# Optimization experiments

Measured on AMD Instinct MI355X. Metric: run time of the kernel, lower is better.

## Reference

```python
import jax, jax.numpy as jnp
import numpy as np

D = 2048
H = 16
HD = 128
INNER = H * HD
EPS = 1e-6


def rmsnorm(x, w):
    var = jnp.mean(x * x, axis=-1, keepdims=True)
    return x * jax.lax.rsqrt(var + EPS) * w


def setup_inputs() -> dict:
    key = jax.random.key(0)
    ks = jax.random.split(key, 10)
    B, T, N_ws, T_corr = 2, 2048, 64, 512
    scale = 1.0 / np.sqrt(D)
    return {
        "hidden_states": jax.random.normal(ks[0], (B, T, D), jnp.float32),
        "workspace": jax.random.normal(ks[1], (B, N_ws, D), jnp.float32),
        "correction_tokens": jax.random.normal(ks[2], (B, T_corr, D), jnp.float32),
        "correction_mask": jax.random.randint(ks[3], (B, T_corr), 0, 2, jnp.int32),
        "ln_q_w": jnp.ones((D,), jnp.float32),
        "ln_kv_w": jnp.ones((D,), jnp.float32),
        "Wq": jax.random.normal(ks[4], (D, INNER), jnp.float32) * scale,
        "Wk": jax.random.normal(ks[5], (D, INNER), jnp.float32) * scale,
        "Wv": jax.random.normal(ks[6], (D, INNER), jnp.float32) * scale,
        "Wo": jax.random.normal(ks[7], (INNER, D), jnp.float32) * scale,
    }


def reference(hidden_states, workspace, correction_tokens, correction_mask,
              ln_q_w, ln_kv_w, Wq, Wk, Wv, Wo):
    B, T, _ = hidden_states.shape
    N_ws = workspace.shape[1]
    # kv context = [workspace ; correction_tokens]
    kv_context = jnp.concatenate([workspace, correction_tokens], axis=1)  # (B, N_kv, D)
    N_kv = kv_context.shape[1]
    ws_mask = jnp.ones((B, N_ws), hidden_states.dtype)
    kv_mask = jnp.concatenate([ws_mask, correction_mask.astype(hidden_states.dtype)], axis=1)  # (B, N_kv)

    h = rmsnorm(hidden_states, ln_q_w)
    kv = rmsnorm(kv_context, ln_kv_w)

    q = (h @ Wq).reshape(B, T, H, HD)        # (B,T,H,hd)
    k = (kv @ Wk).reshape(B, N_kv, H, HD)
    v = (kv @ Wv).reshape(B, N_kv, H, HD)

    scores = jnp.einsum("bthd,bshd->bhts", q, k) / np.sqrt(HD)  # (B,H,T,N_kv)
    mask = (kv_mask != 0)[:, None, None, :]                      # (B,1,1,N_kv)
    scores = jnp.where(mask, scores, -jnp.inf)
    attn = jax.nn.softmax(scores, axis=-1)
    attn = jnp.nan_to_num(attn, nan=0.0)
    # dropout is identity in eval mode
    out = jnp.einsum("bhts,bshd->bthd", attn, v).reshape(B, T, INNER)
    return out @ Wo
```

## Files before the change

### kernel.cpp

```cpp
#include <hip/hip_runtime.h>
#include <hip/hip_bf16.h>
#include <math.h>

typedef __bf16 bf16;
typedef __attribute__((ext_vector_type(8))) __bf16 bf16x8;
typedef __attribute__((ext_vector_type(4))) __bf16 bf16x4;
typedef __attribute__((ext_vector_type(4))) float f32x4;

#define D_DIM 2048
#define NKV   576

__device__ inline void gld_lds16(const void* g, void* l) {
    void* gg = const_cast<void*>(g);
    __builtin_amdgcn_global_load_lds(
        (__attribute__((address_space(1))) void*)gg,
        (__attribute__((address_space(3))) void*)l, 16, 0, 0);
}

__global__ __launch_bounds__(256) void proj_all(
    const bf16* __restrict__ hb, const bf16* __restrict__ kvb,
    const bf16* __restrict__ WqT, const bf16* __restrict__ WkvT,
    bf16* __restrict__ qb, bf16* __restrict__ kvout)
{
    __shared__ __align__(16) bf16 As[128 * 64];
    __shared__ __align__(16) bf16 Bs[128 * 64];

    int id = blockIdx.x;
    const bf16 *A, *B; bf16* C; int ldc, m0, n0;
    if (id < 512) {
        A = hb; B = WqT; C = qb; ldc = 2048;
        m0 = (id >> 4) * 128; n0 = (id & 15) * 128;
    } else {
        id -= 512;
        A = kvb; B = WkvT; C = kvout; ldc = 4096;
        m0 = (id >> 5) * 128; n0 = (id & 31) * 128;
    }
    const int tid = threadIdx.x, lane = tid & 63;
    const int wm = ((tid >> 6) >> 1) * 64, wn = ((tid >> 6) & 1) * 64;
    const int fr = lane & 15, fg = lane >> 4;

    f32x4 acc[4][4] = {};

    for (int k0 = 0; k0 < 2048; k0 += 64) {
#pragma unroll
        for (int p = 0; p < 4; ++p) {
            const int c = p * 256 + tid;
            const int r = c >> 3, cl = (c & 7) ^ (r & 7);
            gld_lds16(A + (long)(m0 + r) * 2048 + k0 + cl * 8, As + c * 8);
            gld_lds16(B + (long)(n0 + r) * 2048 + k0 + cl * 8, Bs + c * 8);
        }
        __syncthreads();
#pragma unroll
        for (int s = 0; s < 2; ++s) {
            const int sl = ((s << 2) + fg) ^ (fr & 7);
            bf16x8 af[4], bg[4];
#pragma unroll
            for (int i = 0; i < 4; ++i)
                af[i] = *(const bf16x8*)(As + (((wm + i * 16 + fr) << 3) + sl) * 8);
#pragma unroll
            for (int j = 0; j < 4; ++j)
                bg[j] = *(const bf16x8*)(Bs + (((wn + j * 16 + fr) << 3) + sl) * 8);
#pragma unroll
            for (int i = 0; i < 4; ++i)
#pragma unroll
                for (int j = 0; j < 4; ++j)
                    acc[i][j] = __builtin_amdgcn_mfma_f32_16x16x32_bf16(
                        af[i], bg[j], acc[i][j], 0, 0, 0);
        }
        __syncthreads();
    }

    const int er = fg * 4;
#pragma unroll
    for (int i = 0; i < 4; ++i)
#pragma unroll
        for (int j = 0; j < 4; ++j) {
            const int n = n0 + wn + j * 16 + fr;
#pragma unroll
            for (int r = 0; r < 4; ++r)
                C[(long)(m0 + wm + i * 16 + er + r) * ldc + n] = (bf16)acc[i][j][r];
        }
}

__global__ __launch_bounds__(256) void gemm_final(
    const bf16* __restrict__ A, const bf16* __restrict__ B, float* __restrict__ C)
{
    __shared__ __align__(16) bf16 As[128 * 64];
    __shared__ __align__(16) bf16 Bs[128 * 64];

    const int m0 = blockIdx.y * 128, n0 = blockIdx.x * 128;
    const int tid = threadIdx.x, lane = tid & 63;
    const int wm = ((tid >> 6) >> 1) * 64, wn = ((tid >> 6) & 1) * 64;
    const int fr = lane & 15, fg = lane >> 4;

    f32x4 acc[4][4] = {};

    for (int k0 = 0; k0 < 2048; k0 += 64) {
#pragma unroll
        for (int p = 0; p < 4; ++p) {
            const int c = p * 256 + tid;
            const int r = c >> 3, cl = (c & 7) ^ (r & 7);
            gld_lds16(A + (long)(m0 + r) * 2048 + k0 + cl * 8, As + c * 8);
            gld_lds16(B + (long)(n0 + r) * 2048 + k0 + cl * 8, Bs + c * 8);
        }
        __syncthreads();
#pragma unroll
        for (int s = 0; s < 2; ++s) {
            const int sl = ((s << 2) + fg) ^ (fr & 7);
            bf16x8 af[4], bg[4];
#pragma unroll
            for (int i = 0; i < 4; ++i)
                af[i] = *(const bf16x8*)(As + (((wm + i * 16 + fr) << 3) + sl) * 8);
#pragma unroll
            for (int j = 0; j < 4; ++j)
                bg[j] = *(const bf16x8*)(Bs + (((wn + j * 16 + fr) << 3) + sl) * 8);
#pragma unroll
            for (int i = 0; i < 4; ++i)
#pragma unroll
                for (int j = 0; j < 4; ++j)
                    acc[i][j] = __builtin_amdgcn_mfma_f32_16x16x32_bf16(
                        af[i], bg[j], acc[i][j], 0, 0, 0);
        }
        __syncthreads();
    }

    const int er = fg * 4;
#pragma unroll
    for (int i = 0; i < 4; ++i)
#pragma unroll
        for (int j = 0; j < 4; ++j) {
            const int n = n0 + wn + j * 16 + fr;
#pragma unroll
            for (int r = 0; r < 4; ++r)
                C[(long)(m0 + wm + i * 16 + er + r) * 2048 + n] = acc[i][j][r];
        }
}

__global__ __launch_bounds__(256) void rmsnorm_all(
    const float* __restrict__ hidden, const float* __restrict__ wsp,
    const float* __restrict__ corr, const float* __restrict__ lnq,
    const float* __restrict__ lnkv, bf16* __restrict__ hb, bf16* __restrict__ kvb)
{
    const int r = blockIdx.x;
    const float* xr; const float* w; bf16* yr;
    if (r < 4096) {
        xr = hidden + (long)r * D_DIM; w = lnq; yr = hb + (long)r * D_DIM;
    } else if (r < 4224) {
        const int rr = r - 4096;
        xr = wsp + (long)rr * D_DIM; w = lnkv;
        yr = kvb + ((long)(rr >> 6) * NKV + (rr & 63)) * D_DIM;
    } else {
        const int rr = r - 4224;
        xr = corr + (long)rr * D_DIM; w = lnkv;
        yr = kvb + ((long)(rr >> 9) * NKV + 64 + (rr & 511)) * D_DIM;
    }
    const int t = threadIdx.x;

    float4 v0 = *(const float4*)(xr + t * 4);
    float4 v1 = *(const float4*)(xr + 1024 + t * 4);
    float ss = v0.x * v0.x + v0.y * v0.y + v0.z * v0.z + v0.w * v0.w
             + v1.x * v1.x + v1.y * v1.y + v1.z * v1.z + v1.w * v1.w;
#pragma unroll
    for (int off = 32; off; off >>= 1) ss += __shfl_xor(ss, off);
    __shared__ float p[4];
    if ((t & 63) == 0) p[t >> 6] = ss;
    __syncthreads();
    const float rs = rsqrtf((p[0] + p[1] + p[2] + p[3]) * (1.0f / 2048.0f) + 1e-6f);

    float4 w0 = *(const float4*)(w + t * 4);
    float4 w1 = *(const float4*)(w + 1024 + t * 4);
    bf16x4 o0 = { (bf16)(v0.x * rs * w0.x), (bf16)(v0.y * rs * w0.y),
                  (bf16)(v0.z * rs * w0.z), (bf16)(v0.w * rs * w0.w) };
    bf16x4 o1 = { (bf16)(v1.x * rs * w1.x), (bf16)(v1.y * rs * w1.y),
                  (bf16)(v1.z * rs * w1.z), (bf16)(v1.w * rs * w1.w) };
    *(bf16x4*)(yr + t * 4) = o0;
    *(bf16x4*)(yr + 1024 + t * 4) = o1;
}

__global__ __launch_bounds__(256) void wcast_t(
    const float* __restrict__ w0, const float* __restrict__ w1,
    const float* __restrict__ w2, const float* __restrict__ w3,
    bf16* __restrict__ o0, bf16* __restrict__ o1,
    bf16* __restrict__ o2, bf16* __restrict__ o3)
{
    const float* in; bf16* out;
    switch (blockIdx.z) {
        case 0:  in = w0; out = o0; break;
        case 1:  in = w1; out = o1; break;
        case 2:  in = w2; out = o2; break;
        default: in = w3; out = o3; break;
    }
    __shared__ float tile[32][33];
    const int t  = threadIdx.x;
    const int r0 = blockIdx.y * 32, c0 = blockIdx.x * 32;
    const int r = t >> 3, c = (t & 7) * 4;
    float4 v = *(const float4*)(in + (long)(r0 + r) * 2048 + c0 + c);
    tile[r][c] = v.x; tile[r][c + 1] = v.y; tile[r][c + 2] = v.z; tile[r][c + 3] = v.w;
    __syncthreads();
    bf16x4 o = { (bf16)tile[c][r], (bf16)tile[c + 1][r],
                 (bf16)tile[c + 2][r], (bf16)tile[c + 3][r] };
    *(bf16x4*)(out + (long)(c0 + r) * 2048 + r0 + c) = o;
}

__global__ __launch_bounds__(256) void vtrans(
    const bf16* __restrict__ kv, bf16* __restrict__ vt)
{
    const int z = blockIdx.z, bb = z >> 4, hh = z & 15;
    __shared__ bf16 tile[32][36];
    const int t  = threadIdx.x;
    const int d0 = blockIdx.x * 32, s0 = blockIdx.y * 32;
    const int r = t >> 3, c = (t & 7) * 4;
    bf16x4 val = *(const bf16x4*)(kv + (long)(bb * NKV + s0 + r) * 4096 + 2048 + hh * 128 + d0 + c);
    tile[r][c] = val[0]; tile[r][c + 1] = val[1];
    tile[r][c + 2] = val[2]; tile[r][c + 3] = val[3];
    __syncthreads();
    bf16x4 o = { tile[c][r], tile[c + 1][r], tile[c + 2][r], tile[c + 3][r] };
    *(bf16x4*)(vt + ((long)z * 128 + d0 + r) * NKV + s0 + c) = o;
}

__global__ __launch_bounds__(256, 4) void flash_attn(
    const bf16* __restrict__ Q, const bf16* __restrict__ KV,
    const bf16* __restrict__ VT, const int* __restrict__ cmask,
    bf16* __restrict__ O)
{
    __shared__ __align__(16) bf16 Ks[64 * 128];
    __shared__ __align__(16) bf16 VTs[128 * 64];

    const int qt = blockIdx.x, h = blockIdx.y, b = blockIdx.z;
    const int tid = threadIdx.x, lane = tid & 63, w = tid >> 6;
    const int fr = lane & 15, fg = lane >> 4;

    const bf16* qbase = Q + ((long)(b * 2048 + qt * 64)) * 2048 + h * 128;
    bf16x8 qf[4];
#pragma unroll
    for (int s = 0; s < 4; ++s)
        qf[s] = *(const bf16x8*)(qbase + (long)(w * 16 + fr) * 2048 + s * 32 + fg * 8);

    float m_r[4], l_r[4];
    f32x4 acc_o[8];
#pragma unroll
    for (int r = 0; r < 4; ++r) { m_r[r] = -3.0e38f; l_r[r] = 0.f; }
#pragma unroll
    for (int j = 0; j < 8; ++j) acc_o[j] = (f32x4){0.f, 0.f, 0.f, 0.f};

    const float scale2 = 0.12752792330124195f;
    const bf16* kbase = KV + (long)b * NKV * 4096 + h * 128;
    const bf16* vbase = VT + ((long)(b * 16 + h)) * 128 * NKV;

    for (int kc = 0; kc < 9; ++kc) {
        const int kv0 = kc * 64;
#pragma unroll
        for (int p = 0; p < 4; ++p) {
            const int c = p * 256 + tid;
            const int r = c >> 4, cs = c & 15, cl = cs ^ (r & 15);
            gld_lds16(kbase + (long)(kv0 + r) * 4096 + cl * 8, Ks + c * 8);
        }
#pragma unroll
        for (int p = 0; p < 4; ++p) {
            const int c = p * 256 + tid;
            const int r = c >> 3, cs = c & 7, cl = cs ^ (r & 7);
            gld_lds16(vbase + (long)r * NKV + kv0 + cl * 8, VTs + c * 8);
        }
        __syncthreads();

        f32x4 acc_s[4] = {};
#pragma unroll
        for (int s = 0; s < 4; ++s) {
#pragma unroll
            for (int j = 0; j < 4; ++j) {
                bf16x8 bg = *(const bf16x8*)(Ks +
                    ((j * 16 + fr) * 16 + ((s * 4 + fg) ^ fr)) * 8);
                acc_s[j] = __builtin_amdgcn_mfma_f32_16x16x32_bf16(qf[s], bg, acc_s[j], 0, 0, 0);
            }
        }

        float bias[4];
#pragma unroll
        for (int j = 0; j < 4; ++j) {
            const int kv = kv0 + j * 16 + fr;
            const bool valid = (kv < 64) || (cmask[b * 512 + kv - 64] != 0);
            bias[j] = valid ? 0.f : -1e30f;
        }
        float s_f[4][4];
        float mc[4] = {-3.0e38f, -3.0e38f, -3.0e38f, -3.0e38f};
#pragma unroll
        for (int j = 0; j < 4; ++j)
#pragma unroll
            for (int r = 0; r < 4; ++r) {
                float v = fmaf(acc_s[j][r], scale2, bias[j]);
                s_f[j][r] = v; mc[r] = fmaxf(mc[r], v);
            }
#pragma unroll
        for (int r = 0; r < 4; ++r) {
            mc[r] = fmaxf(mc[r], __shfl_xor(mc[r], 1));
            mc[r] = fmaxf(mc[r], __shfl_xor(mc[r], 2));
            mc[r] = fmaxf(mc[r], __shfl_xor(mc[r], 4));
            mc[r] = fmaxf(mc[r], __shfl_xor(mc[r], 8));
        }
        float alpha[4];
#pragma unroll
        for (int r = 0; r < 4; ++r) {
            const float mn = fmaxf(m_r[r], mc[r]);
            alpha[r] = __builtin_amdgcn_exp2f(m_r[r] - mn);
            m_r[r] = mn;
        }
        float rs[4] = {0.f, 0.f, 0.f, 0.f};
#pragma unroll
        for (int j = 0; j < 4; ++j)
#pragma unroll
            for (int r = 0; r < 4; ++r) {
                const float pv = __builtin_amdgcn_exp2f(s_f[j][r] - m_r[r]);
                s_f[j][r] = pv; rs[r] += pv;
            }
#pragma unroll
        for (int r = 0; r < 4; ++r) {
            rs[r] += __shfl_xor(rs[r], 1);
            rs[r] += __shfl_xor(rs[r], 2);
            rs[r] += __shfl_xor(rs[r], 4);
            rs[r] += __shfl_xor(rs[r], 8);
            l_r[r] = l_r[r] * alpha[r] + rs[r];
        }
#pragma unroll
        for (int j = 0; j < 8; ++j)
#pragma unroll
            for (int r = 0; r < 4; ++r) acc_o[j][r] *= alpha[r];

        __syncthreads();

        bf16* Ps = Ks;
#pragma unroll
        for (int j = 0; j < 4; ++j)
#pragma unroll
            for (int r = 0; r < 4; ++r)
                Ps[(w * 16 + fg * 4 + r) * 72 + j * 16 + fr] = (bf16)s_f[j][r];

#pragma unroll
        for (int s2 = 0; s2 < 2; ++s2) {
            bf16x8 af = *(const bf16x8*)(Ps + (w * 16 + fr) * 72 + s2 * 32 + fg * 8);
#pragma unroll
            for (int jd = 0; jd < 8; ++jd) {
                bf16x8 bg = *(const bf16x8*)(VTs +
                    ((jd * 16 + fr) * 8 + ((s2 * 4 + fg) ^ (fr & 7))) * 8);
                acc_o[jd] = __builtin_amdgcn_mfma_f32_16x16x32_bf16(af, bg, acc_o[jd], 0, 0, 0);
            }
        }
        __syncthreads();
    }

    bf16* obase = O + ((long)(b * 2048 + qt * 64)) * 2048 + h * 128;
#pragma unroll
    for (int r = 0; r < 4; ++r) {
        const float inv = 1.0f / l_r[r];
        const int row = w * 16 + fg * 4 + r;
#pragma unroll
        for (int jd = 0; jd < 8; ++jd)
            obase[(long)row * 2048 + jd * 16 + fr] = (bf16)(acc_o[jd][r] * inv);
    }
}

extern "C" void kernel_launch(void* const* d_in, const int* in_sizes, int n_in,
                              void* d_out, int out_size, void* d_ws, size_t ws_size,
                              hipStream_t stream)
{
    const float* hidden = (const float*)d_in[0];
    const float* wsp    = (const float*)d_in[1];
    const float* corr   = (const float*)d_in[2];
    const int*   cmask  = (const int*)d_in[3];
    const float* lnq    = (const float*)d_in[4];
    const float* lnkv   = (const float*)d_in[5];
    const float* Wq     = (const float*)d_in[6];
    const float* Wk     = (const float*)d_in[7];
    const float* Wv     = (const float*)d_in[8];
    const float* Wo     = (const float*)d_in[9];
    float* out = (float*)d_out;

    char* ws = (char*)d_ws;
    size_t off = 0;
    auto alloc = [&](size_t sz) { void* p = ws + off; off += (sz + 255) & ~(size_t)255; return p; };

    bf16* WqT   = (bf16*)alloc(2048ull * 2048 * 2);
    bf16* WkvT  = (bf16*)alloc(4096ull * 2048 * 2);
    bf16* WoT   = (bf16*)alloc(2048ull * 2048 * 2);
    bf16* hb    = (bf16*)alloc(4096ull * 2048 * 2);
    bf16* kvb   = (bf16*)alloc(1152ull * 2048 * 2);
    bf16* qb    = (bf16*)alloc(4096ull * 2048 * 2);
    bf16* kvout = (bf16*)alloc(1152ull * 4096 * 2);
    bf16* vtb   = (bf16*)alloc(4096ull * NKV * 2);
    bf16* aob   = (bf16*)alloc(4096ull * 2048 * 2);

    wcast_t<<<dim3(64, 64, 4), 256, 0, stream>>>(
        Wq, Wk, Wv, Wo, WqT, WkvT, WkvT + 2048ull * 2048, WoT);
    rmsnorm_all<<<5248, 256, 0, stream>>>(hidden, wsp, corr, lnq, lnkv, hb, kvb);
    proj_all<<<800, 256, 0, stream>>>(hb, kvb, WqT, WkvT, qb, kvout);
    vtrans<<<dim3(4, 18, 32), 256, 0, stream>>>(kvout, vtb);
    flash_attn<<<dim3(32, 16, 2), 256, 0, stream>>>(qb, kvout, vtb, cmask, aob);
    gemm_final<<<dim3(16, 32), 256, 0, stream>>>(aob, WoT, out);
}
```

Baseline: 331.0 us.

## Fuse weight cast with rmsnorm and fold V transpose into projection epilogue

Merges the weight transpose-cast kernel and the rmsnorm kernel into a single prep launch. The projection GEMM now writes K to its own contiguous buffer and writes V already transposed via an LDS staging tile, which removes the separate vtrans kernel and the extra round trip of V through global memory. This cuts two kernel launches and one intermediate pass, at the cost of a larger shared-memory footprint in the projection kernel and divergent epilogue paths.

```diff
diff --git a/kernel.cpp b/kernel.cpp
--- a/kernel.cpp
+++ b/kernel.cpp
@@ -17,144 +17,53 @@
         (__attribute__((address_space(3))) void*)l, 16, 0, 0);
 }
 
-__global__ __launch_bounds__(256) void proj_all(
-    const bf16* __restrict__ hb, const bf16* __restrict__ kvb,
-    const bf16* __restrict__ WqT, const bf16* __restrict__ WkvT,
-    bf16* __restrict__ qb, bf16* __restrict__ kvout)
-{
-    __shared__ __align__(16) bf16 As[128 * 64];
-    __shared__ __align__(16) bf16 Bs[128 * 64];
-
-    int id = blockIdx.x;
-    const bf16 *A, *B; bf16* C; int ldc, m0, n0;
-    if (id < 512) {
-        A = hb; B = WqT; C = qb; ldc = 2048;
-        m0 = (id >> 4) * 128; n0 = (id & 15) * 128;
-    } else {
-        id -= 512;
-        A = kvb; B = WkvT; C = kvout; ldc = 4096;
-        m0 = (id >> 5) * 128; n0 = (id & 31) * 128;
-    }
-    const int tid = threadIdx.x, lane = tid & 63;
-    const int wm = ((tid >> 6) >> 1) * 64, wn = ((tid >> 6) & 1) * 64;
-    const int fr = lane & 15, fg = lane >> 4;
-
-    f32x4 acc[4][4] = {};
-
-    for (int k0 = 0; k0 < 2048; k0 += 64) {
-#pragma unroll
-        for (int p = 0; p < 4; ++p) {
-            const int c = p * 256 + tid;
-            const int r = c >> 3, cl = (c & 7) ^ (r & 7);
-            gld_lds16(A + (long)(m0 + r) * 2048 + k0 + cl * 8, As + c * 8);
-            gld_lds16(B + (long)(n0 + r) * 2048 + k0 + cl * 8, Bs + c * 8);
-        }
-        __syncthreads();
-#pragma unroll
-        for (int s = 0; s < 2; ++s) {
-            const int sl = ((s << 2) + fg) ^ (fr & 7);
-            bf16x8 af[4], bg[4];
-#pragma unroll
-            for (int i = 0; i < 4; ++i)
-                af[i] = *(const bf16x8*)(As + (((wm + i * 16 + fr) << 3) + sl) * 8);
-#pragma unroll
-            for (int j = 0; j < 4; ++j)
-                bg[j] = *(const bf16x8*)(Bs + (((wn + j * 16 + fr) << 3) + sl) * 8);
-#pragma unroll
-            for (int i = 0; i < 4; ++i)
-#pragma unroll
-                for (int j = 0; j < 4; ++j)
-                    acc[i][j] = __builtin_amdgcn_mfma_f32_16x16x32_bf16(
-                        af[i], bg[j], acc[i][j], 0, 0, 0);
-        }
-        __syncthreads();
-    }
-
-    const int er = fg * 4;
-#pragma unroll
-    for (int i = 0; i < 4; ++i)
-#pragma unroll
-        for (int j = 0; j < 4; ++j) {
-            const int n = n0 + wn + j * 16 + fr;
-#pragma unroll
-            for (int r = 0; r < 4; ++r)
-                C[(long)(m0 + wm + i * 16 + er + r) * ldc + n] = (bf16)acc[i][j][r];
-        }
-}
-
-__global__ __launch_bounds__(256) void gemm_final(
-    const bf16* __restrict__ A, const bf16* __restrict__ B, float* __restrict__ C)
-{
-    __shared__ __align__(16) bf16 As[128 * 64];
-    __shared__ __align__(16) bf16 Bs[128 * 64];
-
-    const int m0 = blockIdx.y * 128, n0 = blockIdx.x * 128;
-    const int tid = threadIdx.x, lane = tid & 63;
-    const int wm = ((tid >> 6) >> 1) * 64, wn = ((tid >> 6) & 1) * 64;
-    const int fr = lane & 15, fg = lane >> 4;
-
-    f32x4 acc[4][4] = {};
-
-    for (int k0 = 0; k0 < 2048; k0 += 64) {
-#pragma unroll
-        for (int p = 0; p < 4; ++p) {
-            const int c = p * 256 + tid;
-            const int r = c >> 3, cl = (c & 7) ^ (r & 7);
-            gld_lds16(A + (long)(m0 + r) * 2048 + k0 + cl * 8, As + c * 8);
-            gld_lds16(B + (long)(n0 + r) * 2048 + k0 + cl * 8, Bs + c * 8);
-        }
-        __syncthreads();
-#pragma unroll
-        for (int s = 0; s < 2; ++s) {
-            const int sl = ((s << 2) + fg) ^ (fr & 7);
-            bf16x8 af[4], bg[4];
-#pragma unroll
-            for (int i = 0; i < 4; ++i)
-                af[i] = *(const bf16x8*)(As + (((wm + i * 16 + fr) << 3) + sl) * 8);
-#pragma unroll
-            for (int j = 0; j < 4; ++j)
-                bg[j] = *(const bf16x8*)(Bs + (((wn + j * 16 + fr) << 3) + sl) * 8);
-#pragma unroll
-            for (int i = 0; i < 4; ++i)
-#pragma unroll
-                for (int j = 0; j < 4; ++j)
-                    acc[i][j] = __builtin_amdgcn_mfma_f32_16x16x32_bf16(
-                        af[i], bg[j], acc[i][j], 0, 0, 0);
-        }
-        __syncthreads();
-    }
-
-    const int er = fg * 4;
-#pragma unroll
-    for (int i = 0; i < 4; ++i)
-#pragma unroll
-        for (int j = 0; j < 4; ++j) {
-            const int n = n0 + wn + j * 16 + fr;
-#pragma unroll
-            for (int r = 0; r < 4; ++r)
-                C[(long)(m0 + wm + i * 16 + er + r) * 2048 + n] = acc[i][j][r];
-        }
-}
-
-__global__ __launch_bounds__(256) void rmsnorm_all(
+__global__ __launch_bounds__(256) void prep(
     const float* __restrict__ hidden, const float* __restrict__ wsp,
     const float* __restrict__ corr, const float* __restrict__ lnq,
-    const float* __restrict__ lnkv, bf16* __restrict__ hb, bf16* __restrict__ kvb)
+    const float* __restrict__ lnkv,
+    const float* __restrict__ Wq, const float* __restrict__ Wk,
+    const float* __restrict__ Wv, const float* __restrict__ Wo,
+    bf16* __restrict__ hb, bf16* __restrict__ kvb,
+    bf16* __restrict__ WqT, bf16* __restrict__ WkvT, bf16* __restrict__ WoT)
 {
-    const int r = blockIdx.x;
+    __shared__ float tile[32][33];
+    __shared__ float p[4];
+    const int id = blockIdx.x, t = threadIdx.x;
+
+    if (id < 16384) {
+        const int wz = id >> 12, wy = (id >> 6) & 63, wx = id & 63;
+        const float* in; bf16* out;
+        switch (wz) {
+            case 0:  in = Wq; out = WqT; break;
+            case 1:  in = Wk; out = WkvT; break;
+            case 2:  in = Wv; out = WkvT + 2048ull * 2048; break;
+            default: in = Wo; out = WoT; break;
+        }
+        const int r0 = wy * 32, c0 = wx * 32;
+        const int r = t >> 3, c = (t & 7) * 4;
+        float4 v = *(const float4*)(in + (long)(r0 + r) * 2048 + c0 + c);
+        tile[r][c] = v.x; tile[r][c + 1] = v.y;
+        tile[r][c + 2] = v.z; tile[r][c + 3] = v.w;
+        __syncthreads();
+        bf16x4 o = { (bf16)tile[c][r], (bf16)tile[c + 1][r],
+                     (bf16)tile[c + 2][r], (bf16)tile[c + 3][r] };
+        *(bf16x4*)(out + (long)(c0 + r) * 2048 + r0 + c) = o;
+        return;
+    }
+
+    const int rr0 = id - 16384;
     const float* xr; const float* w; bf16* yr;
-    if (r < 4096) {
-        xr = hidden + (long)r * D_DIM; w = lnq; yr = hb + (long)r * D_DIM;
-    } else if (r < 4224) {
-        const int rr = r - 4096;
+    if (rr0 < 4096) {
+        xr = hidden + (long)rr0 * D_DIM; w = lnq; yr = hb + (long)rr0 * D_DIM;
+    } else if (rr0 < 4224) {
+        const int rr = rr0 - 4096;
         xr = wsp + (long)rr * D_DIM; w = lnkv;
         yr = kvb + ((long)(rr >> 6) * NKV + (rr & 63)) * D_DIM;
     } else {
-        const int rr = r - 4224;
+        const int rr = rr0 - 4224;
         xr = corr + (long)rr * D_DIM; w = lnkv;
         yr = kvb + ((long)(rr >> 9) * NKV + 64 + (rr & 511)) * D_DIM;
     }
-    const int t = threadIdx.x;
 
     float4 v0 = *(const float4*)(xr + t * 4);
     float4 v1 = *(const float4*)(xr + 1024 + t * 4);
@@ -162,7 +71,6 @@
              + v1.x * v1.x + v1.y * v1.y + v1.z * v1.z + v1.w * v1.w;
 #pragma unroll
     for (int off = 32; off; off >>= 1) ss += __shfl_xor(ss, off);
-    __shared__ float p[4];
     if ((t & 63) == 0) p[t >> 6] = ss;
     __syncthreads();
     const float rs = rsqrtf((p[0] + p[1] + p[2] + p[3]) * (1.0f / 2048.0f) + 1e-6f);
@@ -177,49 +85,155 @@
     *(bf16x4*)(yr + 1024 + t * 4) = o1;
 }
 
-__global__ __launch_bounds__(256) void wcast_t(
-    const float* __restrict__ w0, const float* __restrict__ w1,
-    const float* __restrict__ w2, const float* __restrict__ w3,
-    bf16* __restrict__ o0, bf16* __restrict__ o1,
-    bf16* __restrict__ o2, bf16* __restrict__ o3)
+__global__ __launch_bounds__(256) void proj_all(
+    const bf16* __restrict__ hb, const bf16* __restrict__ kvb,
+    const bf16* __restrict__ WqT, const bf16* __restrict__ WkvT,
+    bf16* __restrict__ qb, bf16* __restrict__ kb, bf16* __restrict__ vtb)
 {
-    const float* in; bf16* out;
-    switch (blockIdx.z) {
-        case 0:  in = w0; out = o0; break;
-        case 1:  in = w1; out = o1; break;
-        case 2:  in = w2; out = o2; break;
-        default: in = w3; out = o3; break;
-    }
-    __shared__ float tile[32][33];
-    const int t  = threadIdx.x;
-    const int r0 = blockIdx.y * 32, c0 = blockIdx.x * 32;
-    const int r = t >> 3, c = (t & 7) * 4;
-    float4 v = *(const float4*)(in + (long)(r0 + r) * 2048 + c0 + c);
-    tile[r][c] = v.x; tile[r][c + 1] = v.y; tile[r][c + 2] = v.z; tile[r][c + 3] = v.w;
+    __shared__ __align__(16) bf16 smem[128 * 132];
+    bf16* As = smem;
+    bf16* Bs = smem + 128 * 64;
+
+    int id = blockIdx.x;
+    const bf16 *A, *B; int m0, n0; bool isQ;
+    if (id < 512) {
+        isQ = true; A = hb; B = WqT;
+        m0 = (id >> 4) * 128; n0 = (id & 15) * 128;
+    } else {
+        id -= 512;
+        isQ = false; A = kvb; B = WkvT;
+        m0 = (id >> 5) * 128; n0 = (id & 31) * 128;
+    }
+    const int tid = threadIdx.x, lane = tid & 63;
+    const int wm = ((tid >> 6) >> 1) * 64, wn = ((tid >> 6) & 1) * 64;
+    const int fr = lane & 15, fg = lane >> 4;
+
+    f32x4 acc[4][4] = {};
+
+    for (int k0 = 0; k0 < 2048; k0 += 64) {
+#pragma unroll
+        for (int p = 0; p < 4; ++p) {
+            const int c = p * 256 + tid;
+            const int r = c >> 3, cl = (c & 7) ^ (r & 7);
+            gld_lds16(A + (long)(m0 + r) * 2048 + k0 + cl * 8, As + c * 8);
+            gld_lds16(B + (long)(n0 + r) * 2048 + k0 + cl * 8, Bs + c * 8);
+        }
+        __syncthreads();
+#pragma unroll
+        for (int s = 0; s < 2; ++s) {
+            const int sl = ((s << 2) + fg) ^ (fr & 7);
+            bf16x8 af[4], bg[4];
+#pragma unroll
+            for (int i = 0; i < 4; ++i)
+                af[i] = *(const bf16x8*)(As + (((wm + i * 16 + fr) << 3) + sl) * 8);
+#pragma unroll
+            for (int j = 0; j < 4; ++j)
+                bg[j] = *(const bf16x8*)(Bs + (((wn + j * 16 + fr) << 3) + sl) * 8);
+#pragma unroll
+            for (int i = 0; i < 4; ++i)
+#pragma unroll
+                for (int j = 0; j < 4; ++j)
+                    acc[i][j] = __builtin_amdgcn_mfma_f32_16x16x32_bf16(
+                        af[i], bg[j], acc[i][j], 0, 0, 0);
+        }
+        __syncthreads();
+    }
+
+    const int er = fg * 4;
+    if (isQ || n0 < 2048) {
+        bf16* C = isQ ? qb : kb;
+        const int ldc = 2048;
+#pragma unroll
+        for (int i = 0; i < 4; ++i)
+#pragma unroll
+            for (int j = 0; j < 4; ++j) {
+                const int n = n0 + wn + j * 16 + fr;
+#pragma unroll
+                for (int r = 0; r < 4; ++r)
+                    C[(long)(m0 + wm + i * 16 + er + r) * ldc + n] = (bf16)acc[i][j][r];
+            }
+        return;
+    }
+
+    const int h = (n0 - 2048) >> 7;
+#pragma unroll
+    for (int i = 0; i < 4; ++i)
+#pragma unroll
+        for (int j = 0; j < 4; ++j) {
+            const int nl = wn + j * 16 + fr;
+#pragma unroll
+            for (int r = 0; r < 4; ++r)
+                smem[nl * 132 + (wm + i * 16 + er + r)] = (bf16)acc[i][j][r];
+        }
     __syncthreads();
-    bf16x4 o = { (bf16)tile[c][r], (bf16)tile[c + 1][r],
-                 (bf16)tile[c + 2][r], (bf16)tile[c + 3][r] };
-    *(bf16x4*)(out + (long)(c0 + r) * 2048 + r0 + c) = o;
-}
-
-__global__ __launch_bounds__(256) void vtrans(
-    const bf16* __restrict__ kv, bf16* __restrict__ vt)
+#pragma unroll
+    for (int p = 0; p < 16; ++p) {
+        const int e = p * 1024 + tid * 4;
+        const int d = e >> 7, mloc = e & 127;
+        bf16x4 val = *(const bf16x4*)(smem + d * 132 + mloc);
+        const int mm = m0 + mloc;
+        const int bb = mm >= NKV;
+        const int s = mm - bb * NKV;
+        *(bf16x4*)(vtb + ((long)((bb * 16 + h) * 128 + d)) * NKV + s) = val;
+    }
+}
+
+__global__ __launch_bounds__(256) void gemm_final(
+    const bf16* __restrict__ A, const bf16* __restrict__ B, float* __restrict__ C)
 {
-    const int z = blockIdx.z, bb = z >> 4, hh = z & 15;
-    __shared__ bf16 tile[32][36];
-    const int t  = threadIdx.x;
-    const int d0 = blockIdx.x * 32, s0 = blockIdx.y * 32;
-    const int r = t >> 3, c = (t & 7) * 4;
-    bf16x4 val = *(const bf16x4*)(kv + (long)(bb * NKV + s0 + r) * 4096 + 2048 + hh * 128 + d0 + c);
-    tile[r][c] = val[0]; tile[r][c + 1] = val[1];
-    tile[r][c + 2] = val[2]; tile[r][c + 3] = val[3];
-    __syncthreads();
-    bf16x4 o = { tile[c][r], tile[c + 1][r], tile[c + 2][r], tile[c + 3][r] };
-    *(bf16x4*)(vt + ((long)z * 128 + d0 + r) * NKV + s0 + c) = o;
+    __shared__ __align__(16) bf16 As[128 * 64];
+    __shared__ __align__(16) bf16 Bs[128 * 64];
+
+    const int m0 = blockIdx.y * 128, n0 = blockIdx.x * 128;
+    const int tid = threadIdx.x, lane = tid & 63;
+    const int wm = ((tid >> 6) >> 1) * 64, wn = ((tid >> 6) & 1) * 64;
+    const int fr = lane & 15, fg = lane >> 4;
+
+    f32x4 acc[4][4] = {};
+
+    for (int k0 = 0; k0 < 2048; k0 += 64) {
+#pragma unroll
+        for (int p = 0; p < 4; ++p) {
+            const int c = p * 256 + tid;
+            const int r = c >> 3, cl = (c & 7) ^ (r & 7);
+            gld_lds16(A + (long)(m0 + r) * 2048 + k0 + cl * 8, As + c * 8);
+            gld_lds16(B + (long)(n0 + r) * 2048 + k0 + cl * 8, Bs + c * 8);
+        }
+        __syncthreads();
+#pragma unroll
+        for (int s = 0; s < 2; ++s) {
+            const int sl = ((s << 2) + fg) ^ (fr & 7);
+            bf16x8 af[4], bg[4];
+#pragma unroll
+            for (int i = 0; i < 4; ++i)
+                af[i] = *(const bf16x8*)(As + (((wm + i * 16 + fr) << 3) + sl) * 8);
+#pragma unroll
+            for (int j = 0; j < 4; ++j)
+                bg[j] = *(const bf16x8*)(Bs + (((wn + j * 16 + fr) << 3) + sl) * 8);
+#pragma unroll
+            for (int i = 0; i < 4; ++i)
+#pragma unroll
+                for (int j = 0; j < 4; ++j)
+                    acc[i][j] = __builtin_amdgcn_mfma_f32_16x16x32_bf16(
+                        af[i], bg[j], acc[i][j], 0, 0, 0);
+        }
+        __syncthreads();
+    }
+
+    const int er = fg * 4;
+#pragma unroll
+    for (int i = 0; i < 4; ++i)
+#pragma unroll
+        for (int j = 0; j < 4; ++j) {
+            const int n = n0 + wn + j * 16 + fr;
+#pragma unroll
+            for (int r = 0; r < 4; ++r)
+                C[(long)(m0 + wm + i * 16 + er + r) * 2048 + n] = acc[i][j][r];
+        }
 }
 
 __global__ __launch_bounds__(256, 4) void flash_attn(
-    const bf16* __restrict__ Q, const bf16* __restrict__ KV,
+    const bf16* __restrict__ Q, const bf16* __restrict__ K,
     const bf16* __restrict__ VT, const int* __restrict__ cmask,
     bf16* __restrict__ O)
 {
@@ -244,7 +258,7 @@
     for (int j = 0; j < 8; ++j) acc_o[j] = (f32x4){0.f, 0.f, 0.f, 0.f};
 
     const float scale2 = 0.12752792330124195f;
-    const bf16* kbase = KV + (long)b * NKV * 4096 + h * 128;
+    const bf16* kbase = K + (long)b * NKV * 2048 + h * 128;
     const bf16* vbase = VT + ((long)(b * 16 + h)) * 128 * NKV;
 
     for (int kc = 0; kc < 9; ++kc) {
@@ -253,7 +267,7 @@
         for (int p = 0; p < 4; ++p) {
             const int c = p * 256 + tid;
             const int r = c >> 4, cs = c & 15, cl = cs ^ (r & 15);
-            gld_lds16(kbase + (long)(kv0 + r) * 4096 + cl * 8, Ks + c * 8);
+            gld_lds16(kbase + (long)(kv0 + r) * 2048 + cl * 8, Ks + c * 8);
         }
 #pragma unroll
         for (int p = 0; p < 4; ++p) {
@@ -384,15 +398,13 @@
     bf16* hb    = (bf16*)alloc(4096ull * 2048 * 2);
     bf16* kvb   = (bf16*)alloc(1152ull * 2048 * 2);
     bf16* qb    = (bf16*)alloc(4096ull * 2048 * 2);
-    bf16* kvout = (bf16*)alloc(1152ull * 4096 * 2);
+    bf16* kb    = (bf16*)alloc(1152ull * 2048 * 2);
     bf16* vtb   = (bf16*)alloc(4096ull * NKV * 2);
     bf16* aob   = (bf16*)alloc(4096ull * 2048 * 2);
 
-    wcast_t<<<dim3(64, 64, 4), 256, 0, stream>>>(
-        Wq, Wk, Wv, Wo, WqT, WkvT, WkvT + 2048ull * 2048, WoT);
-    rmsnorm_all<<<5248, 256, 0, stream>>>(hidden, wsp, corr, lnq, lnkv, hb, kvb);
-    proj_all<<<800, 256, 0, stream>>>(hb, kvb, WqT, WkvT, qb, kvout);
-    vtrans<<<dim3(4, 18, 32), 256, 0, stream>>>(kvout, vtb);
-    flash_attn<<<dim3(32, 16, 2), 256, 0, stream>>>(qb, kvout, vtb, cmask, aob);
+    prep<<<21632, 256, 0, stream>>>(hidden, wsp, corr, lnq, lnkv,
+                                    Wq, Wk, Wv, Wo, hb, kvb, WqT, WkvT, WoT);
+    proj_all<<<800, 256, 0, stream>>>(hb, kvb, WqT, WkvT, qb, kb, vtb);
+    flash_attn<<<dim3(32, 16, 2), 256, 0, stream>>>(qb, kb, vtb, cmask, aob);
     gemm_final<<<dim3(16, 32), 256, 0, stream>>>(aob, WoT, out);
 }
```

After: 324.5 us. No clear change (-2.0%).
